# Performance work log

Hardware: AMD Instinct MI355X
Metric: run time of the kernel (lower is better)

Reference implementation:

```python
import jax, jax.numpy as jnp
import numpy as np

T, D, H, DH, L = 2048, 512, 8, 64, 4
D_OBS, N_ACTS, N_STEPS, DFF = 64, 18, 4096, 2048
EPS = 1e-6


def layer_norm(x, s, b):
    mu = x.mean(-1, keepdims=True)
    var = ((x - mu) ** 2).mean(-1, keepdims=True)
    return (x - mu) * jax.lax.rsqrt(var + EPS) * s + b


def setup_inputs() -> dict:
    key = jax.random.key(0)
    ks = iter(jax.random.split(key, 40))
    rn = lambda shape, sc=0.02: jax.random.normal(next(ks), shape, jnp.float32) * sc
    return dict(
        obs=jax.random.normal(next(ks), (T, D_OBS), jnp.float32),
        rew_p=jax.random.normal(next(ks), (T,), jnp.float32),
        act_p=jax.random.randint(next(ks), (T,), 0, N_ACTS),
        done=jax.random.bernoulli(next(ks), 0.05, (T,)),
        state_obs=jnp.zeros((), jnp.int32),
        state_blocks=jnp.zeros((L, H, DH, DH), jnp.float32),
        w_obs=rn((D_OBS, D)), b_obs=jnp.zeros((D,)),
        emb_act=rn((N_ACTS, D)),
        w_rew=rn((1, D)), b_rew=jnp.zeros((D,)),
        emb_time=rn((N_STEPS, D)),
        ln1_s=jnp.ones((L, D)), ln1_b=jnp.zeros((L, D)),
        w_qkv=rn((L, D, 3 * D)), b_qkv=jnp.zeros((L, 3 * D)),
        w_out=rn((L, D, D)), b_out=jnp.zeros((L, D)),
        ln2_s=jnp.ones((L, D)), ln2_b=jnp.zeros((L, D)),
        w_m1=rn((L, D, DFF)), b_m1=jnp.zeros((L, DFF)),
        w_m2=rn((L, DFF, D)), b_m2=jnp.zeros((L, D)),
        lnf_s=jnp.ones((D,)), lnf_b=jnp.zeros((D,)),
        w_actor=rn((D, N_ACTS), 0.01), b_actor=jnp.zeros((N_ACTS,)),
        w_critic=rn((D, 1)), b_critic=jnp.zeros((1,)),
    )


def _forward(obs, rew_p, state_blocks, w_obs, b_obs, emb_act, w_rew, b_rew, emb_time,
             ln1_s, ln1_b, w_qkv, b_qkv, w_out, b_out, ln2_s, ln2_b,
             w_m1, b_m1, w_m2, b_m2, lnf_s, lnf_b, w_actor, b_actor, w_critic, b_critic,
             act_p, done, state_obs):
    done_i = done.astype(jnp.int32)
    t = jnp.arange(T, dtype=jnp.int32)
    # reset-aware timestep: subtract running max of (time * done) == time at last reset
    time = state_obs + t
    time = time - jax.lax.associative_scan(jnp.maximum, time * done_i)
    x = (obs @ w_obs + b_obs) + emb_act[act_p] + (rew_p[:, None] @ w_rew + b_rew) + emb_time[time]

    # causal-with-resets mask: y can attend x iff y >= x and no done event in (x, y]
    c = jnp.cumsum(done_i)
    mask = (t[:, None] >= t[None, :]) & (c[:, None] == c[None, :])  # [T,T]
    before_first = (c == 0).astype(x.dtype)[None, :, None]      # [1,T,1] tokens before first reset
    after_last = (c == c[-1]).astype(x.dtype)[None, :, None]    # [1,T,1] tokens at/after last reset
    done_any = c[-1] > 0

    states_out = []
    for i in range(L):
        h = layer_norm(x, ln1_s[i], ln1_b[i])
        qkv = (h @ w_qkv[i] + b_qkv[i]).reshape(T, 3, H, DH).transpose(1, 2, 0, 3)  # [3,H,T,DH]
        q, k, v = qkv[0], qkv[1], qkv[2]
        attn = jnp.einsum('htd,hsd->hts', q, k) * mask                 # [H,T,T]
        out = jnp.einsum('hts,hsd->htd', attn, v)
        out = out + jnp.einsum('htd,hde->hte', q * before_first, state_blocks[i])
        s_aft = jnp.einsum('htd,hte->hde', k * after_last, v * after_last)
        states_out.append(jnp.where(done_any, s_aft, state_blocks[i] + s_aft))
        x = x + (out.transpose(1, 0, 2).reshape(T, D) @ w_out[i] + b_out[i])
        h2 = layer_norm(x, ln2_s[i], ln2_b[i])
        x = x + (jax.nn.gelu(h2 @ w_m1[i] + b_m1[i]) @ w_m2[i] + b_m2[i])

    xf = layer_norm(x, lnf_s, lnf_b)
    logits = xf @ w_actor + b_actor
    val = (xf @ w_critic + b_critic)[:, 0]
    return logits, val, time[-1] + 1, jnp.stack(states_out)


def reference(obs, rew_p, act_p, done, state_obs, state_blocks,
              w_obs, b_obs, emb_act, w_rew, b_rew, emb_time,
              ln1_s, ln1_b, w_qkv, b_qkv, w_out, b_out, ln2_s, ln2_b,
              w_m1, b_m1, w_m2, b_m2, lnf_s, lnf_b,
              w_actor, b_actor, w_critic, b_critic):
    return _forward(obs, rew_p, state_blocks, w_obs, b_obs, emb_act, w_rew, b_rew, emb_time,
                    ln1_s, ln1_b, w_qkv, b_qkv, w_out, b_out, ln2_s, ln2_b,
                    w_m1, b_m1, w_m2, b_m2, lnf_s, lnf_b, w_actor, b_actor, w_critic, b_critic,
                    act_p, done, state_obs)
```

## Files before the change

### kernel.cpp

```cpp
#include <hip/hip_runtime.h>
#include <hip/hip_bf16.h>

#define TT 2048
#define DD 512
#define HH 8
#define DH 64
#define LL 4
#define DFF 2048
#define NACT 18
#define TD3 1536

#define OUT_LOGITS 0
#define OUT_VAL    (TT*NACT)
#define OUT_TIME   (OUT_VAL + TT)
#define OUT_STATES (OUT_TIME + 1)

typedef __attribute__((ext_vector_type(8))) short bf16x8;
typedef __attribute__((ext_vector_type(4))) float f32x4;

__device__ inline unsigned short f2bf(float x) {
    __hip_bfloat16 h = __float2bfloat16(x);
    return *reinterpret_cast<unsigned short*>(&h);
}
__device__ inline float bf2f(unsigned short u) {
    __hip_bfloat16 h = *reinterpret_cast<__hip_bfloat16*>(&u);
    return __bfloat162float(h);
}

__global__ __launch_bounds__(256) void k_scan(const unsigned char* __restrict__ done_raw,
                                              const int* __restrict__ state_obs,
                                              int* __restrict__ c_out,
                                              int* __restrict__ t_out,
                                              float* __restrict__ out_time)
{
    __shared__ int sc[TT];
    __shared__ int sm[TT];
    __shared__ int flags[3];
    const int tid = threadIdx.x;
    if (tid < 3) flags[tid] = 0;
    __syncthreads();

    int l0 = 0, l1 = 0, l23 = 0;
    for (int p = tid * 8; p < tid * 8 + 8; ++p) {
        unsigned char b = done_raw[p];
        if (b) {
            int m = p & 3;
            if (m == 0) l0 = 1; else if (m == 1) l1 = 1; else l23 = 1;
        }
    }
    if (l0)  atomicOr(&flags[0], 1);
    if (l1)  atomicOr(&flags[1], 1);
    if (l23) atomicOr(&flags[2], 1);
    __syncthreads();

    int mode;
    if (flags[1] == 0 && flags[2] == 0)      mode = 0;
    else if (flags[0] == 0 && flags[1] == 0) mode = 1;
    else                                     mode = 2;

    const int so = state_obs[0];
    for (int i = tid; i < TT; i += 256) {
        int dn;
        if (mode == 0)      dn = (((const int*)done_raw)[i] != 0);
        else if (mode == 1) dn = (((const float*)done_raw)[i] != 0.0f);
        else                dn = (done_raw[i] != 0);
        sc[i] = dn;
        sm[i] = (so + i) * dn;
    }
    __syncthreads();

    const int NEG = (int)0x80000000;
    for (int off = 1; off < TT; off <<= 1) {
        int ts[8], tm[8];
        #pragma unroll
        for (int j = 0; j < 8; ++j) {
            int idx = tid + j * 256;
            if (idx >= off) { ts[j] = sc[idx - off]; tm[j] = sm[idx - off]; }
            else            { ts[j] = 0;            tm[j] = NEG; }
        }
        __syncthreads();
        #pragma unroll
        for (int j = 0; j < 8; ++j) {
            int idx = tid + j * 256;
            sc[idx] += ts[j];
            sm[idx] = max(sm[idx], tm[j]);
        }
        __syncthreads();
    }

    for (int i = tid; i < TT; i += 256) {
        c_out[i] = sc[i];
        t_out[i] = so + i - sm[i];
    }
    if (tid == 0) out_time[0] = (float)(so + (TT - 1) - sm[TT - 1] + 1);
}

__global__ __launch_bounds__(64) void k_embed_ln(const float* __restrict__ obs,
                                                 const float* __restrict__ rew,
                                                 const int* __restrict__ act,
                                                 const int* __restrict__ tbuf,
                                                 const float* __restrict__ w_obs,
                                                 const float* __restrict__ b_obs,
                                                 const float* __restrict__ emb_act,
                                                 const float* __restrict__ w_rew,
                                                 const float* __restrict__ b_rew,
                                                 const float* __restrict__ emb_time,
                                                 const float* __restrict__ ln_s,
                                                 const float* __restrict__ ln_b,
                                                 float* __restrict__ x,
                                                 unsigned short* __restrict__ hbuf)
{
    const int t = blockIdx.x, lane = threadIdx.x;
    const float* orow = obs + t * 64;
    const float rp = rew[t];
    const float* ea = emb_act + act[t] * DD;
    const float* et = emb_time + tbuf[t] * DD;
    float v[8];
    float sum = 0.f;
    #pragma unroll
    for (int j = 0; j < 8; ++j) {
        const int d = lane + j * 64;
        float a = b_obs[d] + b_rew[d] + ea[d] + rp * w_rew[d] + et[d];
        for (int k = 0; k < 64; ++k) a += orow[k] * w_obs[k * DD + d];
        x[t * DD + d] = a;
        v[j] = a; sum += a;
    }
    #pragma unroll
    for (int off = 32; off >= 1; off >>= 1) sum += __shfl_xor(sum, off);
    const float mu = sum * (1.0f / DD);
    float vs = 0.f;
    #pragma unroll
    for (int j = 0; j < 8; ++j) { float d = v[j] - mu; vs += d * d; }
    #pragma unroll
    for (int off = 32; off >= 1; off >>= 1) vs += __shfl_xor(vs, off);
    const float rs = rsqrtf(vs * (1.0f / DD) + 1e-6f);
    #pragma unroll
    for (int j = 0; j < 8; ++j) {
        int d = lane + j * 64;
        hbuf[t * DD + d] = f2bf((v[j] - mu) * rs * ln_s[d] + ln_b[d]);
    }
}

template<int NS>
__global__ __launch_bounds__(256) void k_red_ln(float* __restrict__ x,
                                                const float* __restrict__ part,
                                                const float* __restrict__ bias,
                                                const float* __restrict__ ln_s,
                                                const float* __restrict__ ln_b,
                                                unsigned short* __restrict__ hbuf)
{
    const int t = blockIdx.x * 4 + (threadIdx.x >> 6);
    const int lane = threadIdx.x & 63;
    float v[8];
    float sum = 0.f;
    #pragma unroll
    for (int j = 0; j < 8; ++j) {
        const int d = lane + j * 64;
        float a = x[(size_t)t * DD + d] + bias[d];
        #pragma unroll
        for (int z = 0; z < NS; ++z)
            a += part[(size_t)z * TT * DD + (size_t)t * DD + d];
        x[(size_t)t * DD + d] = a;
        v[j] = a; sum += a;
    }
    #pragma unroll
    for (int off = 32; off >= 1; off >>= 1) sum += __shfl_xor(sum, off);
    const float mu = sum * (1.0f / DD);
    float vs = 0.f;
    #pragma unroll
    for (int j = 0; j < 8; ++j) { float d = v[j] - mu; vs += d * d; }
    #pragma unroll
    for (int off = 32; off >= 1; off >>= 1) vs += __shfl_xor(vs, off);
    const float rs = rsqrtf(vs * (1.0f / DD) + 1e-6f);
    #pragma unroll
    for (int j = 0; j < 8; ++j) {
        int d = lane + j * 64;
        hbuf[(size_t)t * DD + d] = f2bf((v[j] - mu) * rs * ln_s[d] + ln_b[d]);
    }
}

__global__ __launch_bounds__(256) void k_w2bf_all(const float* __restrict__ w_qkv,
                                                  const float* __restrict__ w_out,
                                                  const float* __restrict__ w_m1,
                                                  const float* __restrict__ w_m2,
                                                  unsigned short* __restrict__ wq_t,
                                                  unsigned short* __restrict__ wo_t,
                                                  unsigned short* __restrict__ wm1_t,
                                                  unsigned short* __restrict__ wm2_t)
{
    __shared__ float tile[32][33];
    const int t = blockIdx.x;
    const int i = blockIdx.y;
    const float* src; unsigned short* dst; int K, N, n0, k0;
    if (t < 768)       { src = w_qkv + (size_t)i * DD * TD3; dst = wq_t  + (size_t)i * TD3 * DD; K = 512;  N = 1536; int l = t;        n0 = (l % 48) * 32; k0 = (l / 48) * 32; }
    else if (t < 1024) { src = w_out + (size_t)i * DD * DD;  dst = wo_t  + (size_t)i * DD * DD;  K = 512;  N = 512;  int l = t - 768;  n0 = (l % 16) * 32; k0 = (l / 16) * 32; }
    else if (t < 2048) { src = w_m1 + (size_t)i * DD * DFF;  dst = wm1_t + (size_t)i * DFF * DD; K = 512;  N = 2048; int l = t - 1024; n0 = (l % 64) * 32; k0 = (l / 64) * 32; }
    else               { src = w_m2 + (size_t)i * DFF * DD;  dst = wm2_t + (size_t)i * DD * DFF; K = 2048; N = 512;  int l = t - 2048; n0 = (l % 16) * 32; k0 = (l / 16) * 32; }
    const int tx = threadIdx.x & 31, ty = threadIdx.x >> 5;
    #pragma unroll
    for (int j = 0; j < 4; ++j)
        tile[ty + 8 * j][tx] = src[(size_t)(k0 + ty + 8 * j) * N + n0 + tx];
    __syncthreads();
    #pragma unroll
    for (int j = 0; j < 4; ++j)
        dst[(size_t)(n0 + ty + 8 * j) * K + k0 + tx] = f2bf(tile[tx][ty + 8 * j]);
}

__device__ inline float gelu_tanh(float x) {
    float x3 = x * x * x;
    return 0.5f * x * (1.0f + tanhf(0.7978845608028654f * (x + 0.044715f * x3)));
}

template<int WM, int WN, int MF, int NF, int KSPLIT, bool GELU_>
__global__ __launch_bounds__(256) void k_gemm4(const unsigned short* __restrict__ A,
                                               const unsigned short* __restrict__ Bt,
                                               const float* __restrict__ bias,
                                               float* __restrict__ Yf,
                                               unsigned short* __restrict__ Yb,
                                               int M, int N, int K)
{
    constexpr int BM = WM * MF * 16;
    constexpr int BN = WN * NF * 16;
    __shared__ __align__(16) unsigned short As[BM][40];
    __shared__ __align__(16) unsigned short Bs[BN][40];

    const int gx = gridDim.x;
    const int nwg = gx * gridDim.y;
    const int bid = blockIdx.y * gx + blockIdx.x;
    const int logical = (bid % 8) * (nwg / 8) + bid / 8;
    const int bm = (logical / gx) * BM, bn = (logical % gx) * BN;

    const int kslice = K / KSPLIT;
    const int kbase = (KSPLIT > 1) ? blockIdx.z * kslice : 0;

    const int tid = threadIdx.x;
    const int lane = tid & 63;
    const int wid = tid >> 6;
    const int wm = wid / WN, wn = wid % WN;
    const int l16 = lane & 15, l4 = lane >> 4;
    const int srow = tid >> 2;
    const int skoff = (tid & 3) * 8;

    f32x4 acc[MF][NF];
    #pragma unroll
    for (int m = 0; m < MF; ++m)
        #pragma unroll
        for (int n = 0; n < NF; ++n)
            acc[m][n] = (f32x4){0.f, 0.f, 0.f, 0.f};

    for (int k0 = kbase; k0 < kbase + kslice; k0 += 32) {
        #pragma unroll
        for (int p = 0; p < BM / 64; ++p)
            *(float4*)&As[srow + p * 64][skoff] =
                *(const float4*)(A + (size_t)(bm + srow + p * 64) * K + k0 + skoff);
        #pragma unroll
        for (int p = 0; p < BN / 64; ++p)
            *(float4*)&Bs[srow + p * 64][skoff] =
                *(const float4*)(Bt + (size_t)(bn + srow + p * 64) * K + k0 + skoff);
        __syncthreads();
        bf16x8 a[MF], b[NF];
        #pragma unroll
        for (int m = 0; m < MF; ++m) a[m] = *(bf16x8*)&As[wm * (MF * 16) + m * 16 + l16][l4 * 8];
        #pragma unroll
        for (int n = 0; n < NF; ++n) b[n] = *(bf16x8*)&Bs[wn * (NF * 16) + n * 16 + l16][l4 * 8];
        #pragma unroll
        for (int m = 0; m < MF; ++m)
            #pragma unroll
            for (int n = 0; n < NF; ++n)
                acc[m][n] = __builtin_amdgcn_mfma_f32_16x16x32_bf16(a[m], b[n], acc[m][n], 0, 0, 0);
        __syncthreads();
    }

    if (KSPLIT > 1) {
        float* P = Yf + (size_t)blockIdx.z * M * N;
        #pragma unroll
        for (int m = 0; m < MF; ++m)
            #pragma unroll
            for (int n = 0; n < NF; ++n) {
                const int col = bn + wn * (NF * 16) + n * 16 + l16;
                #pragma unroll
                for (int r = 0; r < 4; ++r) {
                    const int row = bm + wm * (MF * 16) + m * 16 + l4 * 4 + r;
                    P[(size_t)row * N + col] = acc[m][n][r];
                }
            }
    } else {
        #pragma unroll
        for (int m = 0; m < MF; ++m)
            #pragma unroll
            for (int n = 0; n < NF; ++n) {
                const int col = bn + wn * (NF * 16) + n * 16 + l16;
                const float bz = bias[col];
                #pragma unroll
                for (int r = 0; r < 4; ++r) {
                    const int row = bm + wm * (MF * 16) + m * 16 + l4 * 4 + r;
                    float v = acc[m][n][r] + bz;
                    if (GELU_) v = gelu_tanh(v);
                    Yb[(size_t)row * N + col] = f2bf(v);
                }
            }
    }
}

__global__ __launch_bounds__(256) void k_attn_mfma(const unsigned short* __restrict__ qkv,
                                                   const int* __restrict__ c,
                                                   const float* __restrict__ SB,
                                                   unsigned short* __restrict__ out)
{
    __shared__ __align__(16) unsigned short Qs[64][72];
    __shared__ __align__(16) unsigned short Ks[64][72];
    __shared__ __align__(16) unsigned short VsT[64][72];
    __shared__ __align__(16) unsigned short Ss[64][72];
    __shared__ int cq[64], cs[64];
    const int h = blockIdx.y;
    const int q0 = blockIdx.x * 64;
    const int tid = threadIdx.x;
    const int lane = tid & 63;
    const int wid = tid >> 6;
    const int l16 = lane & 15, l4 = lane >> 4;
    const int wrow = wid * 16;
    const int r1 = tid >> 3, ccol = (tid & 7) * 8;

    *(bf16x8*)&Qs[r1][ccol]      = *(const bf16x8*)(qkv + (size_t)(q0 + r1) * TD3 + h * 64 + ccol);
    *(bf16x8*)&Qs[r1 + 32][ccol] = *(const bf16x8*)(qkv + (size_t)(q0 + r1 + 32) * TD3 + h * 64 + ccol);
    if (tid < 64) cq[tid] = c[q0 + tid];
    __syncthreads();
    const int cq0 = cq[0];

    f32x4 o[4];
    #pragma unroll
    for (int n = 0; n < 4; ++n) o[n] = (f32x4){0.f, 0.f, 0.f, 0.f};

    if (cq0 == 0) {
        for (int i = tid; i < 4096; i += 256) {
            int k = i >> 6, e = i & 63;
            Ss[e][k] = f2bf(SB[(h * 64 + k) * 64 + e]);
        }
        __syncthreads();
        bf16x8 aq0 = *(bf16x8*)&Qs[wrow + l16][l4 * 8];
        bf16x8 aq1 = *(bf16x8*)&Qs[wrow + l16][32 + l4 * 8];
        if (cq[wrow + l16] != 0) {
            aq0 = (bf16x8){0, 0, 0, 0, 0, 0, 0, 0};
            aq1 = (bf16x8){0, 0, 0, 0, 0, 0, 0, 0};
        }
        #pragma unroll
        for (int n = 0; n < 4; ++n) {
            o[n] = __builtin_amdgcn_mfma_f32_16x16x32_bf16(aq0, *(bf16x8*)&Ss[n * 16 + l16][l4 * 8], o[n], 0, 0, 0);
            o[n] = __builtin_amdgcn_mfma_f32_16x16x32_bf16(aq1, *(bf16x8*)&Ss[n * 16 + l16][32 + l4 * 8], o[n], 0, 0, 0);
        }
        __syncthreads();
    }

    for (int st = blockIdx.x; st >= 0; --st) {
        const int s0 = st * 64;
        if (st < (int)blockIdx.x && c[s0 + 63] < cq0) break;

        *(bf16x8*)&Ks[r1][ccol]      = *(const bf16x8*)(qkv + (size_t)(s0 + r1) * TD3 + 512 + h * 64 + ccol);
        *(bf16x8*)&Ks[r1 + 32][ccol] = *(const bf16x8*)(qkv + (size_t)(s0 + r1 + 32) * TD3 + 512 + h * 64 + ccol);
        {
            bf16x8 v1 = *(const bf16x8*)(qkv + (size_t)(s0 + r1) * TD3 + 1024 + h * 64 + ccol);
            bf16x8 v2 = *(const bf16x8*)(qkv + (size_t)(s0 + r1 + 32) * TD3 + 1024 + h * 64 + ccol);
            #pragma unroll
            for (int j = 0; j < 8; ++j) {
                VsT[ccol + j][r1]      = (unsigned short)v1[j];
                VsT[ccol + j][r1 + 32] = (unsigned short)v2[j];
            }
        }
        if (tid < 64) cs[tid] = c[s0 + tid];
        __syncthreads();

        f32x4 s_acc[4];
        #pragma unroll
        for (int n = 0; n < 4; ++n) s_acc[n] = (f32x4){0.f, 0.f, 0.f, 0.f};
        bf16x8 aq0 = *(bf16x8*)&Qs[wrow + l16][l4 * 8];
        bf16x8 aq1 = *(bf16x8*)&Qs[wrow + l16][32 + l4 * 8];
        #pragma unroll
        for (int n = 0; n < 4; ++n) {
            s_acc[n] = __builtin_amdgcn_mfma_f32_16x16x32_bf16(aq0, *(bf16x8*)&Ks[n * 16 + l16][l4 * 8], s_acc[n], 0, 0, 0);
            s_acc[n] = __builtin_amdgcn_mfma_f32_16x16x32_bf16(aq1, *(bf16x8*)&Ks[n * 16 + l16][32 + l4 * 8], s_acc[n], 0, 0, 0);
        }
        #pragma unroll
        for (int n = 0; n < 4; ++n) {
            const int sc_ = n * 16 + l16;
            const int sg = s0 + sc_;
            const int csv = cs[sc_];
            #pragma unroll
            for (int r = 0; r < 4; ++r) {
                const int qrow = wrow + l4 * 4 + r;
                float v = s_acc[n][r];
                if (!((q0 + qrow) >= sg && cq[qrow] == csv)) v = 0.f;
                Ss[qrow][sc_] = f2bf(v);
            }
        }
        bf16x8 as0 = *(bf16x8*)&Ss[wrow + l16][l4 * 8];
        bf16x8 as1 = *(bf16x8*)&Ss[wrow + l16][32 + l4 * 8];
        #pragma unroll
        for (int n = 0; n < 4; ++n) {
            o[n] = __builtin_amdgcn_mfma_f32_16x16x32_bf16(as0, *(bf16x8*)&VsT[n * 16 + l16][l4 * 8], o[n], 0, 0, 0);
            o[n] = __builtin_amdgcn_mfma_f32_16x16x32_bf16(as1, *(bf16x8*)&VsT[n * 16 + l16][32 + l4 * 8], o[n], 0, 0, 0);
        }
        __syncthreads();
    }

    #pragma unroll
    for (int n = 0; n < 4; ++n) {
        const int e = n * 16 + l16;
        #pragma unroll
        for (int r = 0; r < 4; ++r) {
            const int qrow = wrow + l4 * 4 + r;
            out[(size_t)(q0 + qrow) * DD + h * 64 + e] = f2bf(o[n][r]);
        }
    }
}

__global__ __launch_bounds__(256) void k_state_init(const float* __restrict__ SB_all,
                                                    const int* __restrict__ c,
                                                    float* __restrict__ out)
{
    const int idx = blockIdx.x * 256 + threadIdx.x;
    const bool any = c[TT - 1] > 0;
    out[idx] = any ? 0.0f : SB_all[idx];
}

__global__ __launch_bounds__(256) void k_state_acc(const unsigned short* __restrict__ qkv,
                                                   const int* __restrict__ c,
                                                   float* __restrict__ st_out)
{
    const int h = blockIdx.y;
    const int t0 = blockIdx.x * 256;
    const int tid = threadIdx.x;
    const int d = tid >> 2;
    const int e0 = (tid & 3) * 16;
    const int cl = c[TT - 1];
    float acc[16] = {};
    for (int t = t0; t < t0 + 256; ++t) {
        if (c[t] == cl) {
            float kd = bf2f(qkv[(size_t)t * TD3 + 512 + h * 64 + d]);
            const bf16x8* vr = (const bf16x8*)(qkv + (size_t)t * TD3 + 1024 + h * 64 + e0);
            bf16x8 va = vr[0], vb = vr[1];
            #pragma unroll
            for (int e = 0; e < 8; ++e) acc[e]     += kd * bf2f((unsigned short)va[e]);
            #pragma unroll
            for (int e = 0; e < 8; ++e) acc[e + 8] += kd * bf2f((unsigned short)vb[e]);
        }
    }
    #pragma unroll
    for (int e = 0; e < 16; ++e)
        atomicAdd(&st_out[(h * 64 + d) * 64 + e0 + e], acc[e]);
}

__global__ __launch_bounds__(64) void k_heads(const unsigned short* __restrict__ xf,
                                              const float* __restrict__ w_actor,
                                              const float* __restrict__ b_actor,
                                              const float* __restrict__ w_critic,
                                              const float* __restrict__ b_critic,
                                              float* __restrict__ out)
{
    __shared__ float sxf[DD];
    const int t = blockIdx.x, lane = threadIdx.x;
    #pragma unroll
    for (int j = 0; j < 8; ++j) sxf[lane + j * 64] = bf2f(xf[t * DD + lane + j * 64]);
    __syncthreads();
    if (lane < NACT) {
        float a = b_actor[lane];
        for (int k = 0; k < DD; ++k) a += sxf[k] * w_actor[k * NACT + lane];
        out[OUT_LOGITS + t * NACT + lane] = a;
    } else if (lane == NACT) {
        float a = b_critic[0];
        for (int k = 0; k < DD; ++k) a += sxf[k] * w_critic[k];
        out[OUT_VAL + t] = a;
    }
}

extern "C" void kernel_launch(void* const* d_in, const int* in_sizes, int n_in,
                              void* d_out, int out_size, void* d_ws, size_t ws_size,
                              hipStream_t stream)
{
    const float* obs        = (const float*)d_in[0];
    const float* rew_p      = (const float*)d_in[1];
    const int*   act_p      = (const int*)d_in[2];
    const unsigned char* done = (const unsigned char*)d_in[3];
    const int*   state_obs  = (const int*)d_in[4];
    const float* state_blocks = (const float*)d_in[5];
    const float* w_obs      = (const float*)d_in[6];
    const float* b_obs      = (const float*)d_in[7];
    const float* emb_act    = (const float*)d_in[8];
    const float* w_rew      = (const float*)d_in[9];
    const float* b_rew      = (const float*)d_in[10];
    const float* emb_time   = (const float*)d_in[11];
    const float* ln1_s      = (const float*)d_in[12];
    const float* ln1_b      = (const float*)d_in[13];
    const float* w_qkv      = (const float*)d_in[14];
    const float* b_qkv      = (const float*)d_in[15];
    const float* w_out      = (const float*)d_in[16];
    const float* b_out      = (const float*)d_in[17];
    const float* ln2_s      = (const float*)d_in[18];
    const float* ln2_b      = (const float*)d_in[19];
    const float* w_m1       = (const float*)d_in[20];
    const float* b_m1       = (const float*)d_in[21];
    const float* w_m2       = (const float*)d_in[22];
    const float* b_m2       = (const float*)d_in[23];
    const float* lnf_s      = (const float*)d_in[24];
    const float* lnf_b      = (const float*)d_in[25];
    const float* w_actor    = (const float*)d_in[26];
    const float* b_actor    = (const float*)d_in[27];
    const float* w_critic   = (const float*)d_in[28];
    const float* b_critic   = (const float*)d_in[29];

    float* out = (float*)d_out;

    char* ws = (char*)d_ws;
    int*   c_buf = (int*)ws;
    int*   t_buf = c_buf + TT;
    float* x     = (float*)(ws + 16384);
    float* part  = x + (size_t)TT * DD;
    unsigned short* qkvb = (unsigned short*)(part + (size_t)4 * TT * DD);
    unsigned short* hbuf = qkvb + (size_t)TT * TD3;
    unsigned short* aout = hbuf + (size_t)TT * DD;
    unsigned short* mid  = aout + (size_t)TT * DD;
    unsigned short* wq_t = mid + (size_t)TT * DFF;
    unsigned short* wo_t = wq_t + (size_t)LL * TD3 * DD;
    unsigned short* wm1_t = wo_t + (size_t)LL * DD * DD;
    unsigned short* wm2_t = wm1_t + (size_t)LL * DFF * DD;

    k_scan<<<1, 256, 0, stream>>>(done, state_obs, c_buf, t_buf, out + OUT_TIME);

    k_embed_ln<<<TT, 64, 0, stream>>>(obs, rew_p, act_p, t_buf, w_obs, b_obs,
                                      emb_act, w_rew, b_rew, emb_time,
                                      ln1_s, ln1_b, x, hbuf);

    k_state_init<<<LL * HH * DH * DH / 256, 256, 0, stream>>>(state_blocks, c_buf, out + OUT_STATES);

    k_w2bf_all<<<dim3(3072, LL), 256, 0, stream>>>(
        w_qkv, w_out, w_m1, w_m2, wq_t, wo_t, wm1_t, wm2_t);

    for (int i = 0; i < LL; ++i) {
        k_gemm4<2, 2, 4, 4, 1, false><<<dim3(TD3 / 128, TT / 128), 256, 0, stream>>>(
            hbuf, wq_t + (size_t)i * TD3 * DD, b_qkv + i * TD3, nullptr, qkvb, TT, TD3, DD);
        k_attn_mfma<<<dim3(TT / 64, HH), 256, 0, stream>>>(
            qkvb, c_buf, state_blocks + (size_t)i * HH * DH * DH, aout);
        k_state_acc<<<dim3(8, HH), 256, 0, stream>>>(
            qkvb, c_buf, out + OUT_STATES + (size_t)i * HH * DH * DH);
        k_gemm4<4, 1, 2, 4, 2, false><<<dim3(DD / 64, TT / 128, 2), 256, 0, stream>>>(
            aout, wo_t + (size_t)i * DD * DD, nullptr, part, nullptr, TT, DD, DD);
        k_red_ln<2><<<TT / 4, 256, 0, stream>>>(x, part, b_out + i * DD,
                                                ln2_s + i * DD, ln2_b + i * DD, hbuf);
        k_gemm4<2, 2, 4, 4, 1, true><<<dim3(DFF / 128, TT / 128), 256, 0, stream>>>(
            hbuf, wm1_t + (size_t)i * DFF * DD, b_m1 + i * DFF, nullptr, mid, TT, DFF, DD);
        k_gemm4<4, 1, 2, 4, 4, false><<<dim3(DD / 64, TT / 128, 4), 256, 0, stream>>>(
            mid, wm2_t + (size_t)i * DD * DFF, nullptr, part, nullptr, TT, DD, DFF);
        const float* ns = (i < LL - 1) ? ln1_s + (i + 1) * DD : lnf_s;
        const float* nb = (i < LL - 1) ? ln1_b + (i + 1) * DD : lnf_b;
        k_red_ln<4><<<TT / 4, 256, 0, stream>>>(x, part, b_m2 + i * DD, ns, nb, hbuf);
    }

    k_heads<<<TT, 64, 0, stream>>>(hbuf, w_actor, b_actor, w_critic, b_critic, out);
}
```

Before: 681.5 us.

## Use direct global-to-LDS loads in GEMM, fuse heads into final LN, widen state grid

Replaces the templated GEMM with a fixed 128x64 tile kernel that stages A and B through global_load_lds directly into unpadded shared memory, which avoids register staging. QKV and MLP1 now launch twice as many blocks. The actor/critic heads are fused into the last residual-reduce LayerNorm kernel, which drops one launch and the bf16 round trip, and k_state_acc is split over 4x more blocks with more atomics. The unpadded LDS layout may cause bank conflicts on fragment reads, and there is no double buffering.

Result: slower. 782.6 us (+14.8%).

```diff
diff --git a/kernel.cpp b/kernel.cpp
--- a/kernel.cpp
+++ b/kernel.cpp
@@ -25,6 +25,12 @@
 __device__ inline float bf2f(unsigned short u) {
     __hip_bfloat16 h = *reinterpret_cast<__hip_bfloat16*>(&u);
     return __bfloat162float(h);
+}
+
+__device__ __forceinline__ void gload_lds16(const unsigned short* g, unsigned short* l) {
+    __builtin_amdgcn_global_load_lds(
+        (const __attribute__((address_space(1))) void*)g,
+        (__attribute__((address_space(3))) void*)l, 16, 0, 0);
 }
 
 __global__ __launch_bounds__(256) void k_scan(const unsigned char* __restrict__ done_raw,
@@ -141,15 +147,22 @@
     }
 }
 
-template<int NS>
+template<int NS, bool HEADS>
 __global__ __launch_bounds__(256) void k_red_ln(float* __restrict__ x,
                                                 const float* __restrict__ part,
                                                 const float* __restrict__ bias,
                                                 const float* __restrict__ ln_s,
                                                 const float* __restrict__ ln_b,
-                                                unsigned short* __restrict__ hbuf)
-{
-    const int t = blockIdx.x * 4 + (threadIdx.x >> 6);
+                                                unsigned short* __restrict__ hbuf,
+                                                const float* __restrict__ w_actor,
+                                                const float* __restrict__ b_actor,
+                                                const float* __restrict__ w_critic,
+                                                const float* __restrict__ b_critic,
+                                                float* __restrict__ out)
+{
+    __shared__ float xfs[4][DD];
+    const int w4 = threadIdx.x >> 6;
+    const int t = blockIdx.x * 4 + w4;
     const int lane = threadIdx.x & 63;
     float v[8];
     float sum = 0.f;
@@ -160,7 +173,7 @@
         #pragma unroll
         for (int z = 0; z < NS; ++z)
             a += part[(size_t)z * TT * DD + (size_t)t * DD + d];
-        x[(size_t)t * DD + d] = a;
+        if (!HEADS) x[(size_t)t * DD + d] = a;
         v[j] = a; sum += a;
     }
     #pragma unroll
@@ -175,7 +188,20 @@
     #pragma unroll
     for (int j = 0; j < 8; ++j) {
         int d = lane + j * 64;
-        hbuf[(size_t)t * DD + d] = f2bf((v[j] - mu) * rs * ln_s[d] + ln_b[d]);
+        float xf = (v[j] - mu) * rs * ln_s[d] + ln_b[d];
+        if (HEADS) xfs[w4][d] = xf;
+        else       hbuf[(size_t)t * DD + d] = f2bf(xf);
+    }
+    if (HEADS) {
+        if (lane < NACT) {
+            float a = b_actor[lane];
+            for (int k = 0; k < DD; ++k) a += xfs[w4][k] * w_actor[k * NACT + lane];
+            out[OUT_LOGITS + t * NACT + lane] = a;
+        } else if (lane == NACT) {
+            float a = b_critic[0];
+            for (int k = 0; k < DD; ++k) a += xfs[w4][k] * w_critic[k];
+            out[OUT_VAL + t] = a;
+        }
     }
 }
 
@@ -211,24 +237,22 @@
     return 0.5f * x * (1.0f + tanhf(0.7978845608028654f * (x + 0.044715f * x3)));
 }
 
-template<int WM, int WN, int MF, int NF, int KSPLIT, bool GELU_>
-__global__ __launch_bounds__(256) void k_gemm4(const unsigned short* __restrict__ A,
+template<int KSPLIT, bool GELU_>
+__global__ __launch_bounds__(256) void k_gemm5(const unsigned short* __restrict__ A,
                                                const unsigned short* __restrict__ Bt,
                                                const float* __restrict__ bias,
                                                float* __restrict__ Yf,
                                                unsigned short* __restrict__ Yb,
                                                int M, int N, int K)
 {
-    constexpr int BM = WM * MF * 16;
-    constexpr int BN = WN * NF * 16;
-    __shared__ __align__(16) unsigned short As[BM][40];
-    __shared__ __align__(16) unsigned short Bs[BN][40];
+    __shared__ __align__(16) unsigned short As[128][32];
+    __shared__ __align__(16) unsigned short Bs[64][32];
 
     const int gx = gridDim.x;
     const int nwg = gx * gridDim.y;
     const int bid = blockIdx.y * gx + blockIdx.x;
     const int logical = (bid % 8) * (nwg / 8) + bid / 8;
-    const int bm = (logical / gx) * BM, bn = (logical % gx) * BN;
+    const int bm = (logical / gx) * 128, bn = (logical % gx) * 64;
 
     const int kslice = K / KSPLIT;
     const int kbase = (KSPLIT > 1) ? blockIdx.z * kslice : 0;
@@ -236,37 +260,38 @@
     const int tid = threadIdx.x;
     const int lane = tid & 63;
     const int wid = tid >> 6;
-    const int wm = wid / WN, wn = wid % WN;
     const int l16 = lane & 15, l4 = lane >> 4;
-    const int srow = tid >> 2;
-    const int skoff = (tid & 3) * 8;
-
-    f32x4 acc[MF][NF];
-    #pragma unroll
-    for (int m = 0; m < MF; ++m)
-        #pragma unroll
-        for (int n = 0; n < NF; ++n)
+    const int lr = lane >> 2;
+    const int lc = (lane & 3) * 8;
+
+    const unsigned short* gA0 = A  + (size_t)(bm + wid * 16 + lr) * K + kbase + lc;
+    const unsigned short* gA1 = A  + (size_t)(bm + 64 + wid * 16 + lr) * K + kbase + lc;
+    const unsigned short* gB  = Bt + (size_t)(bn + wid * 16 + lr) * K + kbase + lc;
+    unsigned short* lA0 = &As[wid * 16][0];
+    unsigned short* lA1 = &As[64 + wid * 16][0];
+    unsigned short* lB  = &Bs[wid * 16][0];
+
+    f32x4 acc[2][4];
+    #pragma unroll
+    for (int m = 0; m < 2; ++m)
+        #pragma unroll
+        for (int n = 0; n < 4; ++n)
             acc[m][n] = (f32x4){0.f, 0.f, 0.f, 0.f};
 
-    for (int k0 = kbase; k0 < kbase + kslice; k0 += 32) {
-        #pragma unroll
-        for (int p = 0; p < BM / 64; ++p)
-            *(float4*)&As[srow + p * 64][skoff] =
-                *(const float4*)(A + (size_t)(bm + srow + p * 64) * K + k0 + skoff);
-        #pragma unroll
-        for (int p = 0; p < BN / 64; ++p)
-            *(float4*)&Bs[srow + p * 64][skoff] =
-                *(const float4*)(Bt + (size_t)(bn + srow + p * 64) * K + k0 + skoff);
-        __syncthreads();
-        bf16x8 a[MF], b[NF];
-        #pragma unroll
-        for (int m = 0; m < MF; ++m) a[m] = *(bf16x8*)&As[wm * (MF * 16) + m * 16 + l16][l4 * 8];
-        #pragma unroll
-        for (int n = 0; n < NF; ++n) b[n] = *(bf16x8*)&Bs[wn * (NF * 16) + n * 16 + l16][l4 * 8];
-        #pragma unroll
-        for (int m = 0; m < MF; ++m)
-            #pragma unroll
-            for (int n = 0; n < NF; ++n)
+    for (int k0 = 0; k0 < kslice; k0 += 32) {
+        gload_lds16(gA0 + k0, lA0);
+        gload_lds16(gA1 + k0, lA1);
+        gload_lds16(gB + k0, lB);
+        __syncthreads();
+        bf16x8 a[2], b[4];
+        a[0] = *(bf16x8*)&As[wid * 32 + l16][l4 * 8];
+        a[1] = *(bf16x8*)&As[wid * 32 + 16 + l16][l4 * 8];
+        #pragma unroll
+        for (int n = 0; n < 4; ++n) b[n] = *(bf16x8*)&Bs[n * 16 + l16][l4 * 8];
+        #pragma unroll
+        for (int m = 0; m < 2; ++m)
+            #pragma unroll
+            for (int n = 0; n < 4; ++n)
                 acc[m][n] = __builtin_amdgcn_mfma_f32_16x16x32_bf16(a[m], b[n], acc[m][n], 0, 0, 0);
         __syncthreads();
     }
@@ -274,26 +299,26 @@
     if (KSPLIT > 1) {
         float* P = Yf + (size_t)blockIdx.z * M * N;
         #pragma unroll
-        for (int m = 0; m < MF; ++m)
-            #pragma unroll
-            for (int n = 0; n < NF; ++n) {
-                const int col = bn + wn * (NF * 16) + n * 16 + l16;
+        for (int m = 0; m < 2; ++m)
+            #pragma unroll
+            for (int n = 0; n < 4; ++n) {
+                const int col = bn + n * 16 + l16;
                 #pragma unroll
                 for (int r = 0; r < 4; ++r) {
-                    const int row = bm + wm * (MF * 16) + m * 16 + l4 * 4 + r;
+                    const int row = bm + wid * 32 + m * 16 + l4 * 4 + r;
                     P[(size_t)row * N + col] = acc[m][n][r];
                 }
             }
     } else {
         #pragma unroll
-        for (int m = 0; m < MF; ++m)
-            #pragma unroll
-            for (int n = 0; n < NF; ++n) {
-                const int col = bn + wn * (NF * 16) + n * 16 + l16;
+        for (int m = 0; m < 2; ++m)
+            #pragma unroll
+            for (int n = 0; n < 4; ++n) {
+                const int col = bn + n * 16 + l16;
                 const float bz = bias[col];
                 #pragma unroll
                 for (int r = 0; r < 4; ++r) {
-                    const int row = bm + wm * (MF * 16) + m * 16 + l4 * 4 + r;
+                    const int row = bm + wid * 32 + m * 16 + l4 * 4 + r;
                     float v = acc[m][n][r] + bz;
                     if (GELU_) v = gelu_tanh(v);
                     Yb[(size_t)row * N + col] = f2bf(v);
@@ -427,13 +452,13 @@
                                                    float* __restrict__ st_out)
 {
     const int h = blockIdx.y;
-    const int t0 = blockIdx.x * 256;
+    const int t0 = blockIdx.x * 64;
     const int tid = threadIdx.x;
     const int d = tid >> 2;
     const int e0 = (tid & 3) * 16;
     const int cl = c[TT - 1];
     float acc[16] = {};
-    for (int t = t0; t < t0 + 256; ++t) {
+    for (int t = t0; t < t0 + 64; ++t) {
         if (c[t] == cl) {
             float kd = bf2f(qkv[(size_t)t * TD3 + 512 + h * 64 + d]);
             const bf16x8* vr = (const bf16x8*)(qkv + (size_t)t * TD3 + 1024 + h * 64 + e0);
@@ -447,29 +472,6 @@
     #pragma unroll
     for (int e = 0; e < 16; ++e)
         atomicAdd(&st_out[(h * 64 + d) * 64 + e0 + e], acc[e]);
-}
-
-__global__ __launch_bounds__(64) void k_heads(const unsigned short* __restrict__ xf,
-                                              const float* __restrict__ w_actor,
-                                              const float* __restrict__ b_actor,
-                                              const float* __restrict__ w_critic,
-                                              const float* __restrict__ b_critic,
-                                              float* __restrict__ out)
-{
-    __shared__ float sxf[DD];
-    const int t = blockIdx.x, lane = threadIdx.x;
-    #pragma unroll
-    for (int j = 0; j < 8; ++j) sxf[lane + j * 64] = bf2f(xf[t * DD + lane + j * 64]);
-    __syncthreads();
-    if (lane < NACT) {
-        float a = b_actor[lane];
-        for (int k = 0; k < DD; ++k) a += sxf[k] * w_actor[k * NACT + lane];
-        out[OUT_LOGITS + t * NACT + lane] = a;
-    } else if (lane == NACT) {
-        float a = b_critic[0];
-        for (int k = 0; k < DD; ++k) a += sxf[k] * w_critic[k];
-        out[OUT_VAL + t] = a;
-    }
 }
 
 extern "C" void kernel_launch(void* const* d_in, const int* in_sizes, int n_in,
@@ -535,24 +537,27 @@
         w_qkv, w_out, w_m1, w_m2, wq_t, wo_t, wm1_t, wm2_t);
 
     for (int i = 0; i < LL; ++i) {
-        k_gemm4<2, 2, 4, 4, 1, false><<<dim3(TD3 / 128, TT / 128), 256, 0, stream>>>(
+        k_gemm5<1, false><<<dim3(TD3 / 64, TT / 128), 256, 0, stream>>>(
             hbuf, wq_t + (size_t)i * TD3 * DD, b_qkv + i * TD3, nullptr, qkvb, TT, TD3, DD);
         k_attn_mfma<<<dim3(TT / 64, HH), 256, 0, stream>>>(
             qkvb, c_buf, state_blocks + (size_t)i * HH * DH * DH, aout);
-        k_state_acc<<<dim3(8, HH), 256, 0, stream>>>(
+        k_state_acc<<<dim3(32, HH), 256, 0, stream>>>(
             qkvb, c_buf, out + OUT_STATES + (size_t)i * HH * DH * DH);
-        k_gemm4<4, 1, 2, 4, 2, false><<<dim3(DD / 64, TT / 128, 2), 256, 0, stream>>>(
+        k_gemm5<2, false><<<dim3(DD / 64, TT / 128, 2), 256, 0, stream>>>(
             aout, wo_t + (size_t)i * DD * DD, nullptr, part, nullptr, TT, DD, DD);
-        k_red_ln<2><<<TT / 4, 256, 0, stream>>>(x, part, b_out + i * DD,
-                                                ln2_s + i * DD, ln2_b + i * DD, hbuf);
-        k_gemm4<2, 2, 4, 4, 1, true><<<dim3(DFF / 128, TT / 128), 256, 0, stream>>>(
+        k_red_ln<2, false><<<TT / 4, 256, 0, stream>>>(x, part, b_out + i * DD,
+            ln2_s + i * DD, ln2_b + i * DD, hbuf, nullptr, nullptr, nullptr, nullptr, nullptr);
+        k_gemm5<1, true><<<dim3(DFF / 64, TT / 128), 256, 0, stream>>>(
             hbuf, wm1_t + (size_t)i * DFF * DD, b_m1 + i * DFF, nullptr, mid, TT, DFF, DD);
-        k_gemm4<4, 1, 2, 4, 4, false><<<dim3(DD / 64, TT / 128, 4), 256, 0, stream>>>(
+        k_gemm5<4, false><<<dim3(DD / 64, TT / 128, 4), 256, 0, stream>>>(
             mid, wm2_t + (size_t)i * DD * DFF, nullptr, part, nullptr, TT, DD, DFF);
-        const float* ns = (i < LL - 1) ? ln1_s + (i + 1) * DD : lnf_s;
-        const float* nb = (i < LL - 1) ? ln1_b + (i + 1) * DD : lnf_b;
-        k_red_ln<4><<<TT / 4, 256, 0, stream>>>(x, part, b_m2 + i * DD, ns, nb, hbuf);
-    }
-
-    k_heads<<<TT, 64, 0, stream>>>(hbuf, w_actor, b_actor, w_critic, b_critic, out);
-}
+        if (i < LL - 1) {
+            k_red_ln<4, false><<<TT / 4, 256, 0, stream>>>(x, part, b_m2 + i * DD,
+                ln1_s + (i + 1) * DD, ln1_b + (i + 1) * DD, hbuf,
+                nullptr, nullptr, nullptr, nullptr, nullptr);
+        } else {
+            k_red_ln<4, true><<<TT / 4, 256, 0, stream>>>(x, part, b_m2 + i * DD,
+                lnf_s, lnf_b, hbuf, w_actor, b_actor, w_critic, b_critic, out);
+        }
+    }
+}
```
